# Kernel tuning notes

Hardware: AMD Instinct MI355X
Metric: run time of the kernel (lower is better)

## Reference

```python
import jax, jax.numpy as jnp
import numpy as np

DIM = 128
HEADS = 8
HD = DIM // HEADS          # 16
KS = 8                     # neighborhood kernel size
STRIDE = 2                 # GNA query-group stride
DIL = 2                    # dilation


def axis_indices(L, k, s, d):
    """Per-axis neighborhood indices [L, k] for dilated, strided, edge-clamped NA.

    Queries are grouped in blocks of `s`; every query in a block shares the
    window of the block's center query (GNA 'stride'). Dilation partitions the
    axis into `d` sub-grids; the window lives on the center query's sub-grid
    and is clamped so it never leaves the axis (natten-style sliding window).
    """
    idx = np.zeros((L, k), dtype=np.int32)
    for i in range(L):
        ic = min((i // s) * s + (s - 1) // 2, L - 1)   # group-center query
        r = ic % d                                      # sub-grid (residue)
        Lsub = (L - r + d - 1) // d                     # sub-grid length
        ii = ic // d                                    # index within sub-grid
        start = min(max(ii - (k - 1) // 2, 0), max(Lsub - k, 0))
        for j in range(k):
            idx[i, j] = r + d * min(start + j, Lsub - 1)
    return idx


def setup_inputs() -> dict:
    key = jax.random.key(0)
    ks = jax.random.split(key, 5)
    x = jax.random.normal(ks[0], (1, DIM, 96, 96), jnp.float32)
    # depthwise-grouped qkv conv: Conv2d(dim, 3*dim, 3, 1, 1, groups=dim)
    qkv_w = jax.random.normal(ks[1], (3 * DIM, 1, 3, 3), jnp.float32) * 0.1
    qkv_b = jax.random.normal(ks[2], (3 * DIM,), jnp.float32) * 0.02
    # 1x1 projection: Conv2d(dim, dim, 1)
    proj_w = jax.random.normal(ks[3], (DIM, DIM, 1, 1), jnp.float32) * (DIM ** -0.5)
    proj_b = jax.random.normal(ks[4], (DIM,), jnp.float32) * 0.02
    return {"x": x, "qkv_w": qkv_w, "qkv_b": qkv_b, "proj_w": proj_w, "proj_b": proj_b}


def reference(x, qkv_w, qkv_b, proj_w, proj_b):
    B, C, H, W = x.shape
    # grouped (groups=C) 3x3 conv producing q,k,v
    qkv = jax.lax.conv_general_dilated(
        x, qkv_w, window_strides=(1, 1), padding=[(1, 1), (1, 1)],
        dimension_numbers=("NCHW", "OIHW", "NCHW"), feature_group_count=C)
    qkv = qkv + qkv_b[None, :, None, None]
    qkv = qkv.reshape(B, 3, C, H, W)

    def to_heads(t):  # b c h w -> b h w nh hd
        return t.reshape(B, HEADS, HD, H, W).transpose(0, 3, 4, 1, 2)

    q = to_heads(qkv[:, 0])
    k = to_heads(qkv[:, 1])
    v = to_heads(qkv[:, 2])

    scale = HD ** -0.5
    ri = jnp.asarray(axis_indices(H, KS, STRIDE, DIL))  # [H, KS]
    ci = jnp.asarray(axis_indices(W, KS, STRIDE, DIL))  # [W, KS]
    R = ri[:, :, None, None]       # [H, KS, 1, 1]
    Cc = ci[None, None, :, :]      # [1, 1, W, KS]
    k_win = k[:, R, Cc]            # [B, H, KS, W, KS, nh, hd]
    v_win = v[:, R, Cc]

    logits = jnp.einsum("bijnd,bipjqnd->bijnpq", q * scale, k_win)
    attn = jax.nn.softmax(logits.reshape(B, H, W, HEADS, KS * KS), axis=-1)
    attn = attn.reshape(B, H, W, HEADS, KS, KS)
    out = jnp.einsum("bijnpq,bipjqnd->bijnd", attn, v_win)

    out = out.transpose(0, 3, 4, 1, 2).reshape(B, C, H, W)  # b h w nh hd -> b c h w
    out = jnp.einsum("bchw,oc->bohw", out, proj_w[:, :, 0, 0]) + proj_b[None, :, None, None]
    return out
```

## Files before the change

kernel.cpp:

```cpp
#include <hip/hip_runtime.h>
#include <hip/hip_bf16.h>

#define HH   96
#define WW   96
#define NPIX 9216
#define CH   128
#define NH   8
#define HD   16
#define KS   8

#define NPOS    120
#define KVPITCH 40
#define PMPITCH 392
#define WTPITCH 132

__device__ __forceinline__ unsigned short f2bf(float f) {
    __hip_bfloat16 b = __float2bfloat16(f);
    union { __hip_bfloat16 b; unsigned short u; } cv; cv.b = b; return cv.u;
}
__device__ __forceinline__ float bf2f(unsigned short h) {
    return __uint_as_float(((unsigned)h) << 16);
}
__device__ __forceinline__ void u4_to_f8(uint4 u, float* f) {
    f[0] = __uint_as_float(u.x << 16); f[1] = __uint_as_float(u.x & 0xffff0000u);
    f[2] = __uint_as_float(u.y << 16); f[3] = __uint_as_float(u.y & 0xffff0000u);
    f[4] = __uint_as_float(u.z << 16); f[5] = __uint_as_float(u.z & 0xffff0000u);
    f[6] = __uint_as_float(u.w << 16); f[7] = __uint_as_float(u.w & 0xffff0000u);
}

__global__ __launch_bounds__(256) void conv_pm_kernel(
    const float* __restrict__ x,
    const float* __restrict__ w,
    const float* __restrict__ bias,
    unsigned short* __restrict__ qkv_pm)
{
    __shared__ unsigned short ldst[24 * PMPITCH];

    const int row = blockIdx.x >> 2;
    const int q   = blockIdx.x & 3;
    const int j0q = q * 24;
    const int tid = threadIdx.x;
    const int g   = tid >> 1;
    const int sh  = tid & 1;
    const int j0  = j0q + sh * 12;

    const float* xg = x + g * NPIX;

    float xr[3][14];
    #pragma unroll
    for (int dr = 0; dr < 3; ++dr) {
        const int r = row + dr - 1;
        if (r >= 0 && r < HH) {
            #pragma unroll
            for (int m = 0; m < 14; ++m) {
                const int j = j0 + m - 1;
                xr[dr][m] = (j >= 0 && j < WW) ? xg[r * WW + j] : 0.f;
            }
        } else {
            #pragma unroll
            for (int m = 0; m < 14; ++m) xr[dr][m] = 0.f;
        }
    }

    #pragma unroll
    for (int dt = 0; dt < 3; ++dt) {
        const int o = 3 * g + dt;
        float w9[9];
        #pragma unroll
        for (int k = 0; k < 9; ++k) w9[k] = w[o * 9 + k];
        const float b = bias[o];

        #pragma unroll
        for (int px = 0; px < 12; ++px) {
            float acc = b;
            #pragma unroll
            for (int kh = 0; kh < 3; ++kh)
                #pragma unroll
                for (int kw = 0; kw < 3; ++kw)
                    acc += xr[kh][px + kw] * w9[kh * 3 + kw];
            ldst[(sh * 12 + px) * PMPITCH + o] = f2bf(acc);
        }
    }

    __syncthreads();

    #pragma unroll
    for (int it = 0; it < 5; ++it) {
        const int idx = it * 256 + tid;
        if (idx < 1152) {
            const int px = idx / 48;
            const int c8 = idx - px * 48;
            const int o  = c8 * 8;
            const uint4 v = *(const uint4*)&ldst[px * PMPITCH + o];
            const int t = o >> 7, c = o & 127;
            *(uint4*)(qkv_pm + ((size_t)t * NPIX + row * WW + j0q + px) * CH + c) = v;
        }
    }
}

__global__ __launch_bounds__(256) void attn_proj_kernel(
    const unsigned short* __restrict__ qkv_pm,
    const float* __restrict__ pw,
    const float* __restrict__ pb,
    float* __restrict__ out)
{
    __shared__ union SM {
        unsigned short kv[2][NPOS * KVPITCH];
        float          al[32 * 17];
    } sm;
    __shared__ unsigned short wT[32 * WTPITCH];

    const int tid = threadIdx.x;
    const int seg = blockIdx.x;
    const int hp  = blockIdx.y;
    const int i   = seg / 6;
    const int j0  = (seg - i * 6) * 16;
    const int rs     = 2 * min(max(i / 2 - 3, 0), 40);
    const int cs_min = 2 * min(max(j0 / 2 - 3, 0), 40);

    #pragma unroll
    for (int it = 0; it < 16; ++it) {
        const int idx = it * 256 + tid;
        const int o   = idx >> 5;
        const int cl  = idx & 31;
        wT[cl * WTPITCH + o] = f2bf(pw[o * CH + hp * 32 + cl]);
    }

    #pragma unroll
    for (int it = 0; it < 4; ++it) {
        const int idx = it * 256 + tid;
        if (idx < 960) {
            const int kvsel = idx / 480;
            const int rem   = idx - kvsel * 480;
            const int pos   = rem >> 2;
            const int sub   = rem & 3;
            const int p     = pos / 15;
            const int cc    = pos - p * 15;
            const int pixg  = (rs + 2 * p) * WW + cs_min + 2 * cc;
            *(uint4*)&sm.kv[kvsel][pos * KVPITCH + sub * 8] =
                *(const uint4*)(qkv_pm + ((size_t)(1 + kvsel) * NPIX + pixg) * CH
                                + hp * 32 + sub * 8);
        }
    }

    const int lane  = tid & 63;
    const int wave  = tid >> 6;
    const int r     = lane >> 3;
    const int hh    = (lane >> 2) & 1;
    const int px    = wave * 4 + (lane & 3);
    const int h     = hp * 2 + hh;
    const int pix   = seg * 16 + px;
    const int j     = j0 + px;
    const int ci0   = (2 * min(max(j / 2 - 3, 0), 40) - cs_min) >> 1;

    float qr[HD];
    {
        const unsigned short* qp = qkv_pm + (size_t)pix * CH + h * HD;
        u4_to_f8(*(const uint4*)qp, qr);
        u4_to_f8(*(const uint4*)(qp + 8), qr + 8);
        #pragma unroll
        for (int d = 0; d < HD; ++d) qr[d] *= 0.25f;
    }

    __syncthreads();

    const int posr = r * 15 + ci0;
    float lg[KS];
    float m = -1e30f;
    #pragma unroll
    for (int q = 0; q < KS; ++q) {
        const unsigned short* kp = &sm.kv[0][(posr + q) * KVPITCH + hh * HD];
        float kf[HD];
        u4_to_f8(*(const uint4*)kp, kf);
        u4_to_f8(*(const uint4*)(kp + 8), kf + 8);
        float acc = 0.f;
        #pragma unroll
        for (int d = 0; d < HD; ++d) acc += qr[d] * kf[d];
        lg[q] = acc;
        m = fmaxf(m, acc);
    }

    float s = 0.f;
    #pragma unroll
    for (int q = 0; q < KS; ++q) { lg[q] = __expf(lg[q] - m); s += lg[q]; }

    float o[HD];
    #pragma unroll
    for (int d = 0; d < HD; ++d) o[d] = 0.f;
    #pragma unroll
    for (int q = 0; q < KS; ++q) {
        const unsigned short* vp = &sm.kv[1][(posr + q) * KVPITCH + hh * HD];
        float vf[HD];
        u4_to_f8(*(const uint4*)vp, vf);
        u4_to_f8(*(const uint4*)(vp + 8), vf + 8);
        const float wgt = lg[q];
        #pragma unroll
        for (int d = 0; d < HD; ++d) o[d] += wgt * vf[d];
    }

    #pragma unroll
    for (int mask = 8; mask <= 32; mask <<= 1) {
        const float m2 = __shfl_xor(m, mask);
        const float s2 = __shfl_xor(s, mask);
        const float mn = fmaxf(m, m2);
        const float ea = __expf(m - mn);
        const float eb = __expf(m2 - mn);
        s = s * ea + s2 * eb;
        #pragma unroll
        for (int d = 0; d < HD; ++d) {
            const float o2 = __shfl_xor(o[d], mask);
            o[d] = o[d] * ea + o2 * eb;
        }
        m = mn;
    }
    const float inv = 1.f / s;

    __syncthreads();
    sm.al[(hh * 16 + 2 * r)     * 17 + px] = o[2 * r]     * inv;
    sm.al[(hh * 16 + 2 * r + 1) * 17 + px] = o[2 * r + 1] * inv;
    __syncthreads();

    const int og  = tid >> 4;
    const int px2 = tid & 15;
    const int o0  = og * 8;

    float acc[8];
    if (hp == 0) {
        #pragma unroll
        for (int u = 0; u < 8; ++u) acc[u] = pb[o0 + u];
    } else {
        #pragma unroll
        for (int u = 0; u < 8; ++u) acc[u] = 0.f;
    }

    #pragma unroll
    for (int c = 0; c < 32; ++c) {
        const float a = sm.al[c * 17 + px2];
        float wf[8];
        const unsigned short* wp = &wT[c * WTPITCH + o0];
        u4_to_f8(*(const uint4*)wp, wf);
        #pragma unroll
        for (int u = 0; u < 8; ++u) acc[u] += a * wf[u];
    }

    const int pix2 = seg * 16 + px2;
    #pragma unroll
    for (int u = 0; u < 8; ++u)
        atomicAdd(out + (size_t)(o0 + u) * NPIX + pix2, acc[u]);
}

extern "C" void kernel_launch(void* const* d_in, const int* in_sizes, int n_in,
                              void* d_out, int out_size, void* d_ws, size_t ws_size,
                              hipStream_t stream)
{
    const float* x      = (const float*)d_in[0];
    const float* qkv_w  = (const float*)d_in[1];
    const float* qkv_b  = (const float*)d_in[2];
    const float* proj_w = (const float*)d_in[3];
    const float* proj_b = (const float*)d_in[4];
    float* out = (float*)d_out;

    unsigned short* qkv_pm = (unsigned short*)d_ws;

    conv_pm_kernel  <<<384, 256, 0, stream>>>(x, qkv_w, qkv_b, qkv_pm);
    attn_proj_kernel<<<dim3(576, 4), 256, 0, stream>>>(qkv_pm, proj_w, proj_b, out);
}
```

Baseline: 107.1 us.

## Process all heads per block to drop atomics in fused projection

Each block now handles 8 pixels across all 8 heads (512 threads) instead of 16 pixels across a pair of heads, so the 1x1 projection sees all 128 channels locally. Output is written with plain stores instead of atomicAdd, which removes the atomic traffic and the need for a zeroed output. Projection weights are read as fp32 straight from global memory in float4s rather than being staged transposed in LDS as bf16. The cost is a larger per-block KV tile (88 positions x 128 channels) and more redundant K/V loads from overlapping windows with narrower pixel segments.

```diff
diff --git a/kernel.cpp b/kernel.cpp
--- a/kernel.cpp
+++ b/kernel.cpp
@@ -9,17 +9,14 @@
 #define HD   16
 #define KS   8
 
-#define NPOS    120
-#define KVPITCH 40
+#define NPOS8   88
+#define KVP     136
+#define APITCH  132
 #define PMPITCH 392
-#define WTPITCH 132
 
 __device__ __forceinline__ unsigned short f2bf(float f) {
     __hip_bfloat16 b = __float2bfloat16(f);
     union { __hip_bfloat16 b; unsigned short u; } cv; cv.b = b; return cv.u;
-}
-__device__ __forceinline__ float bf2f(unsigned short h) {
-    return __uint_as_float(((unsigned)h) << 16);
 }
 __device__ __forceinline__ void u4_to_f8(uint4 u, float* f) {
     f[0] = __uint_as_float(u.x << 16); f[1] = __uint_as_float(u.x & 0xffff0000u);
@@ -98,60 +95,47 @@
     }
 }
 
-__global__ __launch_bounds__(256) void attn_proj_kernel(
+__global__ __launch_bounds__(512) void attn_proj_kernel(
     const unsigned short* __restrict__ qkv_pm,
     const float* __restrict__ pw,
     const float* __restrict__ pb,
     float* __restrict__ out)
 {
     __shared__ union SM {
-        unsigned short kv[2][NPOS * KVPITCH];
-        float          al[32 * 17];
+        unsigned short kv[2][NPOS8 * KVP];
+        float          al[8 * APITCH];
     } sm;
-    __shared__ unsigned short wT[32 * WTPITCH];
 
     const int tid = threadIdx.x;
     const int seg = blockIdx.x;
-    const int hp  = blockIdx.y;
-    const int i   = seg / 6;
-    const int j0  = (seg - i * 6) * 16;
+    const int i   = seg / 12;
+    const int j0  = (seg - i * 12) * 8;
     const int rs     = 2 * min(max(i / 2 - 3, 0), 40);
     const int cs_min = 2 * min(max(j0 / 2 - 3, 0), 40);
 
     #pragma unroll
-    for (int it = 0; it < 16; ++it) {
-        const int idx = it * 256 + tid;
-        const int o   = idx >> 5;
-        const int cl  = idx & 31;
-        wT[cl * WTPITCH + o] = f2bf(pw[o * CH + hp * 32 + cl]);
-    }
-
-    #pragma unroll
-    for (int it = 0; it < 4; ++it) {
-        const int idx = it * 256 + tid;
-        if (idx < 960) {
-            const int kvsel = idx / 480;
-            const int rem   = idx - kvsel * 480;
-            const int pos   = rem >> 2;
-            const int sub   = rem & 3;
-            const int p     = pos / 15;
-            const int cc    = pos - p * 15;
+    for (int it = 0; it < 6; ++it) {
+        const int idx = it * 512 + tid;
+        if (idx < 2816) {
+            const int kvsel = idx / 1408;
+            const int rem   = idx - kvsel * 1408;
+            const int pos   = rem >> 4;
+            const int sub   = rem & 15;
+            const int p     = pos / 11;
+            const int cc    = pos - p * 11;
             const int pixg  = (rs + 2 * p) * WW + cs_min + 2 * cc;
-            *(uint4*)&sm.kv[kvsel][pos * KVPITCH + sub * 8] =
-                *(const uint4*)(qkv_pm + ((size_t)(1 + kvsel) * NPIX + pixg) * CH
-                                + hp * 32 + sub * 8);
-        }
-    }
-
-    const int lane  = tid & 63;
-    const int wave  = tid >> 6;
-    const int r     = lane >> 3;
-    const int hh    = (lane >> 2) & 1;
-    const int px    = wave * 4 + (lane & 3);
-    const int h     = hp * 2 + hh;
-    const int pix   = seg * 16 + px;
-    const int j     = j0 + px;
-    const int ci0   = (2 * min(max(j / 2 - 3, 0), 40) - cs_min) >> 1;
+            *(uint4*)&sm.kv[kvsel][pos * KVP + sub * 8] =
+                *(const uint4*)(qkv_pm + ((size_t)(1 + kvsel) * NPIX + pixg) * CH + sub * 8);
+        }
+    }
+
+    const int lane = tid & 63;
+    const int h    = tid >> 6;
+    const int px   = lane & 7;
+    const int r    = lane >> 3;
+    const int pix  = seg * 8 + px;
+    const int j    = j0 + px;
+    const int ci0  = (2 * min(max(j / 2 - 3, 0), 40) - cs_min) >> 1;
 
     float qr[HD];
     {
@@ -164,12 +148,12 @@
 
     __syncthreads();
 
-    const int posr = r * 15 + ci0;
+    const int posr = r * 11 + ci0;
     float lg[KS];
     float m = -1e30f;
     #pragma unroll
     for (int q = 0; q < KS; ++q) {
-        const unsigned short* kp = &sm.kv[0][(posr + q) * KVPITCH + hh * HD];
+        const unsigned short* kp = &sm.kv[0][(posr + q) * KVP + h * HD];
         float kf[HD];
         u4_to_f8(*(const uint4*)kp, kf);
         u4_to_f8(*(const uint4*)(kp + 8), kf + 8);
@@ -189,7 +173,7 @@
     for (int d = 0; d < HD; ++d) o[d] = 0.f;
     #pragma unroll
     for (int q = 0; q < KS; ++q) {
-        const unsigned short* vp = &sm.kv[1][(posr + q) * KVPITCH + hh * HD];
+        const unsigned short* vp = &sm.kv[1][(posr + q) * KVP + h * HD];
         float vf[HD];
         u4_to_f8(*(const uint4*)vp, vf);
         u4_to_f8(*(const uint4*)(vp + 8), vf + 8);
@@ -216,37 +200,25 @@
     const float inv = 1.f / s;
 
     __syncthreads();
-    sm.al[(hh * 16 + 2 * r)     * 17 + px] = o[2 * r]     * inv;
-    sm.al[(hh * 16 + 2 * r + 1) * 17 + px] = o[2 * r + 1] * inv;
-    __syncthreads();
-
-    const int og  = tid >> 4;
-    const int px2 = tid & 15;
-    const int o0  = og * 8;
-
-    float acc[8];
-    if (hp == 0) {
-        #pragma unroll
-        for (int u = 0; u < 8; ++u) acc[u] = pb[o0 + u];
-    } else {
-        #pragma unroll
-        for (int u = 0; u < 8; ++u) acc[u] = 0.f;
-    }
-
-    #pragma unroll
-    for (int c = 0; c < 32; ++c) {
-        const float a = sm.al[c * 17 + px2];
-        float wf[8];
-        const unsigned short* wp = &wT[c * WTPITCH + o0];
-        u4_to_f8(*(const uint4*)wp, wf);
-        #pragma unroll
-        for (int u = 0; u < 8; ++u) acc[u] += a * wf[u];
-    }
-
-    const int pix2 = seg * 16 + px2;
-    #pragma unroll
-    for (int u = 0; u < 8; ++u)
-        atomicAdd(out + (size_t)(o0 + u) * NPIX + pix2, acc[u]);
+    sm.al[px * APITCH + h * HD + 2 * r]     = o[2 * r]     * inv;
+    sm.al[px * APITCH + h * HD + 2 * r + 1] = o[2 * r + 1] * inv;
+    __syncthreads();
+
+    const int px2 = tid & 7;
+    const int o0  = (tid >> 3) * 2;
+
+    float a0 = pb[o0], a1 = pb[o0 + 1];
+    #pragma unroll
+    for (int c0 = 0; c0 < CH; c0 += 4) {
+        const float4 av = *(const float4*)&sm.al[px2 * APITCH + c0];
+        const float4 w0 = *(const float4*)(pw + (size_t)(o0)     * CH + c0);
+        const float4 w1 = *(const float4*)(pw + (size_t)(o0 + 1) * CH + c0);
+        a0 += av.x * w0.x + av.y * w0.y + av.z * w0.z + av.w * w0.w;
+        a1 += av.x * w1.x + av.y * w1.y + av.z * w1.z + av.w * w1.w;
+    }
+
+    out[(size_t)(o0)     * NPIX + seg * 8 + px2] = a0;
+    out[(size_t)(o0 + 1) * NPIX + seg * 8 + px2] = a1;
 }
 
 extern "C" void kernel_launch(void* const* d_in, const int* in_sizes, int n_in,
@@ -263,5 +235,5 @@
     unsigned short* qkv_pm = (unsigned short*)d_ws;
 
     conv_pm_kernel  <<<384, 256, 0, stream>>>(x, qkv_w, qkv_b, qkv_pm);
-    attn_proj_kernel<<<dim3(576, 4), 256, 0, stream>>>(qkv_pm, proj_w, proj_b, out);
-}
+    attn_proj_kernel<<<1152, 512, 0, stream>>>(qkv_pm, proj_w, proj_b, out);
+}
```

Result: no change. 107.8 us (+0.7%).
